# Performance work log

Hardware: AMD Instinct MI355X
Metric: run time of the kernel (lower is better)

## Reference

```python
import jax, jax.numpy as jnp
import numpy as np

BLOCK_SIZE = 256
N_EMBD = 256
HEAD_SIZE = 64


def setup_inputs() -> dict:
    key = jax.random.key(0)
    k1, k2, k3, k4, k5 = jax.random.split(key, 5)
    B, T = 256, 256
    x = jax.random.normal(k1, (B, T, N_EMBD), dtype=jnp.float32)
    # nn.Linear(n_embd, head_size, bias=False) weights, stored as [in, out] for x @ W
    s = 1.0 / np.sqrt(N_EMBD)
    Wk = jax.random.uniform(k2, (N_EMBD, HEAD_SIZE), minval=-s, maxval=s, dtype=jnp.float32)
    Wq = jax.random.uniform(k3, (N_EMBD, HEAD_SIZE), minval=-s, maxval=s, dtype=jnp.float32)
    Wv = jax.random.uniform(k4, (N_EMBD, HEAD_SIZE), minval=-s, maxval=s, dtype=jnp.float32)
    rel_pos_embedding = 0.02 * jax.random.normal(k5, (2 * BLOCK_SIZE - 1, HEAD_SIZE), dtype=jnp.float32)
    return {"x": x, "Wk": Wk, "Wq": Wq, "Wv": Wv, "rel_pos_embedding": rel_pos_embedding}


def reference(x, Wk, Wq, Wv, rel_pos_embedding):
    B, T, C = x.shape
    H = Wk.shape[-1]
    k = x @ Wk  # [B,T,H]
    q = x @ Wq  # [B,T,H]
    v = x @ Wv  # [B,T,H]
    # content scores (scaled); note: position scores are NOT scaled, matching original
    content = jnp.einsum('bth,bsh->bts', q, k) * (H ** -0.5)  # [B,T,T]
    # relative position indices: j - i + (block_size - 1)
    idx = jnp.arange(T)[None, :] - jnp.arange(T)[:, None] + (BLOCK_SIZE - 1)  # [T,T]
    rel_emb = rel_pos_embedding[idx]  # [T,T,H]
    position = jnp.einsum('bth,tsh->bts', q, rel_emb)  # [B,T,T]
    wei = content + position
    causal = jnp.tril(jnp.ones((T, T), dtype=bool))
    wei = jnp.where(causal[None, :, :], wei, -jnp.inf)
    wei = jax.nn.softmax(wei, axis=-1)
    # dropout omitted (eval mode / deterministic reference)
    out = jnp.einsum('bts,bsh->bth', wei, v)  # [B,T,H]
    return out
```

## Files before the change

### kernel.cpp

```cpp
#include <hip/hip_runtime.h>

#define BB 256
#define TT 256
#define CC 256
#define HH 64

typedef _Float16 half8 __attribute__((ext_vector_type(8)));
typedef _Float16 half4 __attribute__((ext_vector_type(4)));
typedef __fp16 fp16x2 __attribute__((ext_vector_type(2)));
typedef float floatx4 __attribute__((ext_vector_type(4)));

__global__ __launch_bounds__(256) void prep(
    const float* __restrict__ rpe,
    const float* __restrict__ Wk, const float* __restrict__ Wq, const float* __restrict__ Wv,
    _Float16* __restrict__ rpeh, _Float16* __restrict__ WT)
{
    const int bid = blockIdx.x, tid = threadIdx.x;
    if (bid < 64) {
        const int i = bid * 256 + tid;
        rpeh[i] = (_Float16)rpe[i];
    } else {
        const int wsel = (bid - 64) >> 6;
        const int n    = (bid - 64) & 63;
        const float* W = wsel == 0 ? Wk : (wsel == 1 ? Wq : Wv);
        WT[(size_t)(wsel * 64 + n) * 256 + tid] = (_Float16)W[tid * HH + n];
    }
}

__device__ __forceinline__ int slot_width(int w) {
    const int j = w >> 1;
    return (j < 2) ? 72 : (32 * j + 40);
}
__device__ __forceinline__ int slot_off(int w) {
    const int j = w >> 1;
    const int V = (j < 2) ? 72 : (32 * j + 40);
    const int S = (j == 0) ? 0 : (j == 1) ? 72 : (16 * j * j + 24 * j + 32);
    return 32 * S + (w & 1) * 16 * V;
}

__global__ __launch_bounds__(1024, 4) void fused(
    const float* __restrict__ x, const _Float16* __restrict__ WT,
    const _Float16* __restrict__ rpeh, float* __restrict__ out)
{
    __shared__ _Float16 lds[75264];
    _Float16* Klds = lds;
    _Float16* VT   = lds + 18432;
    _Float16* pool = lds + 35328;

    const int tid  = threadIdx.x;
    const int b    = blockIdx.x;
    const int w    = tid >> 6;
    const int lane = tid & 63;
    const int quad = lane >> 4;
    const int l    = lane & 15;

    union H8 { half8 v; fp16x2 p[4]; };
    const float4* xg = reinterpret_cast<const float4*>(x);
    const int row0g = b * 256 + w * 16;

    floatx4 acc[12];
#pragma unroll
    for (int nt = 0; nt < 12; ++nt) acc[nt] = (floatx4){0.f, 0.f, 0.f, 0.f};

#pragma unroll
    for (int c = 0; c < 2; ++c) {
#pragma unroll
        for (int i = 0; i < 3; ++i) {
            const int gi  = tid + i * 1024;
            const int row = gi >> 4;
            const int g   = gi & 15;
            *(half8*)&pool[row * 136 + g * 8] =
                *(const half8*)(WT + (size_t)row * 256 + c * 128 + g * 8);
        }
        __syncthreads();

        float4 xa[4][2];
#pragma unroll
        for (int kk = 0; kk < 4; ++kk) {
            const size_t base = (size_t)(row0g + l) * 64 + c * 32 + kk * 8 + quad * 2;
            xa[kk][0] = xg[base];
            xa[kk][1] = xg[base + 1];
        }
#pragma unroll
        for (int kk = 0; kk < 4; ++kk) {
            H8 u;
            u.p[0] = __builtin_amdgcn_cvt_pkrtz(xa[kk][0].x, xa[kk][0].y);
            u.p[1] = __builtin_amdgcn_cvt_pkrtz(xa[kk][0].z, xa[kk][0].w);
            u.p[2] = __builtin_amdgcn_cvt_pkrtz(xa[kk][1].x, xa[kk][1].y);
            u.p[3] = __builtin_amdgcn_cvt_pkrtz(xa[kk][1].z, xa[kk][1].w);
#pragma unroll
            for (int nt = 0; nt < 12; ++nt) {
                const half8 bf = *(const half8*)&pool[(nt * 16 + l) * 136 + kk * 32 + quad * 8];
                acc[nt] = __builtin_amdgcn_mfma_f32_16x16x32_f16(u.v, bf, acc[nt], 0, 0, 0);
            }
        }
        __syncthreads();
    }

    {
        const int trw = w * 16;
#pragma unroll
        for (int nt = 0; nt < 4; ++nt) {
#pragma unroll
            for (int r = 0; r < 4; ++r)
                Klds[(trw + quad * 4 + r) * 72 + nt * 16 + l] = (_Float16)(acc[nt][r] * 0.125f);
            half4 vv;
            vv[0] = (_Float16)acc[nt + 8][0];
            vv[1] = (_Float16)acc[nt + 8][1];
            vv[2] = (_Float16)acc[nt + 8][2];
            vv[3] = (_Float16)acc[nt + 8][3];
            *(half4*)&VT[(nt * 16 + l) * 264 + trw + quad * 4] = vv;
        }
    }
    __syncthreads();

    _Float16* wh = pool + slot_off(w);
    const int Vw = slot_width(w);
    const int tile  = w;
    const int tw    = tile * 16;
    const int stmax = tile;
    const int cmax  = tile >> 1;
    const int dtmin = 15 - tile;

    half8 qf0, qf1;
    {
#pragma unroll
        for (int nt = 0; nt < 4; ++nt)
#pragma unroll
            for (int r = 0; r < 4; ++r)
                wh[(quad * 4 + r) * Vw + nt * 16 + l] = (_Float16)acc[nt + 4][r];
        qf0 = *(const half8*)&wh[l * Vw + quad * 8];
        qf1 = *(const half8*)&wh[l * Vw + 32 + quad * 8];
    }

#pragma unroll
    for (int dt = 0; dt < 16; ++dt) {
        if (dt >= dtmin) {
            const _Float16* rp = rpeh + (size_t)(dt * 16 + l) * HH + quad * 8;
            const half8 bf0 = *(const half8*)rp;
            const half8 bf1 = *(const half8*)(rp + 32);
            floatx4 z = {0.f, 0.f, 0.f, 0.f};
            z = __builtin_amdgcn_mfma_f32_16x16x32_f16(qf0, bf0, z, 0, 0, 0);
            const floatx4 pacc = __builtin_amdgcn_mfma_f32_16x16x32_f16(qf1, bf1, z, 0, 0, 0);
            if (dt == dtmin) {
#pragma unroll
                for (int r = 0; r < 4; ++r) {
                    const int row = quad * 4 + r;
                    const int s   = l + row - 15;
                    if (s >= 0) wh[row * Vw + s] = (_Float16)pacc[r];
                }
            } else {
#pragma unroll
                for (int r = 0; r < 4; ++r) {
                    const int row = quad * 4 + r;
                    const int s   = dt * 16 + l + tw + row - 255;
                    wh[row * Vw + s] = (_Float16)pacc[r];
                }
            }
        }
    }

    floatx4 sacc[16];
#pragma unroll
    for (int st = 0; st < 16; ++st) {
        if (st <= stmax) {
            const _Float16* kp = &Klds[(st * 16 + l) * 72 + quad * 8];
            const half8 kf0 = *(const half8*)kp;
            const half8 kf1 = *(const half8*)(kp + 32);
            floatx4 z = {0.f, 0.f, 0.f, 0.f};
            z = __builtin_amdgcn_mfma_f32_16x16x32_f16(qf0, kf0, z, 0, 0, 0);
            sacc[st] = __builtin_amdgcn_mfma_f32_16x16x32_f16(qf1, kf1, z, 0, 0, 0);
        }
    }

    float sums[4] = {0.f, 0.f, 0.f, 0.f};
#pragma unroll
    for (int st = 0; st < 16; ++st) {
        if (st < stmax) {
            const int s = l + 16 * st;
#pragma unroll
            for (int r = 0; r < 4; ++r) {
                const int row = quad * 4 + r;
                const float e = __expf(sacc[st][r] + (float)wh[row * Vw + s]);
                sums[r] += e;
                wh[row * Vw + s] = (_Float16)e;
            }
        }
    }
    {
        const int s = l + 16 * stmax;
#pragma unroll
        for (int r = 0; r < 4; ++r) {
            const int row = quad * 4 + r;
            float e = 0.f;
            if (l <= row) e = __expf(sacc[stmax][r] + (float)wh[row * Vw + s]);
            sums[r] += e;
            wh[row * Vw + s] = (_Float16)e;
        }
    }
    if ((tile & 1) == 0) {
        const int s = l + 16 * (stmax + 1);
#pragma unroll
        for (int r = 0; r < 4; ++r) wh[(quad * 4 + r) * Vw + s] = (_Float16)0.f;
    }

    float inv_r[4];
#pragma unroll
    for (int r = 0; r < 4; ++r) {
        float sum = sums[r];
        sum += __shfl_xor(sum, 1);
        sum += __shfl_xor(sum, 2);
        sum += __shfl_xor(sum, 4);
        sum += __shfl_xor(sum, 8);
        inv_r[r] = 1.0f / sum;
    }

    floatx4 oacc[4] = {{0.f,0.f,0.f,0.f},{0.f,0.f,0.f,0.f},
                       {0.f,0.f,0.f,0.f},{0.f,0.f,0.f,0.f}};
#pragma unroll
    for (int c = 0; c < 8; ++c) {
        if (c <= cmax) {
            const half8 af = *(const half8*)&wh[l * Vw + c * 32 + quad * 8];
#pragma unroll
            for (int ht = 0; ht < 4; ++ht) {
                const half8 vf = *(const half8*)&VT[(ht * 16 + l) * 264 + c * 32 + quad * 8];
                oacc[ht] = __builtin_amdgcn_mfma_f32_16x16x32_f16(af, vf, oacc[ht], 0, 0, 0);
            }
        }
    }

#pragma unroll
    for (int ht = 0; ht < 4; ++ht) {
#pragma unroll
        for (int r = 0; r < 4; ++r) {
            const int t = tw + quad * 4 + r;
            out[(size_t)(b * TT + t) * HH + ht * 16 + l] = oacc[ht][r] * inv_r[r];
        }
    }
}

extern "C" void kernel_launch(void* const* d_in, const int* in_sizes, int n_in,
                              void* d_out, int out_size, void* d_ws, size_t ws_size,
                              hipStream_t stream) {
    const float* x   = (const float*)d_in[0];
    const float* Wk  = (const float*)d_in[1];
    const float* Wq  = (const float*)d_in[2];
    const float* Wv  = (const float*)d_in[3];
    const float* rpe = (const float*)d_in[4];
    float* out = (float*)d_out;

    _Float16* rpeh = (_Float16*)d_ws;
    _Float16* WT   = rpeh + 256 * HH;

    prep<<<dim3(256), dim3(256), 0, stream>>>(rpe, Wk, Wq, Wv, rpeh, WT);
    fused<<<dim3(BB), dim3(1024), 0, stream>>>(x, WT, rpeh, out);
}
```

Baseline: 131.9 us.

## Balance causal attention work across waves by splitting long query tiles

Reassigns the triangular causal workload so each wave processes its own tile up to nine key tiles and, for waves 0-7, also the tail key tiles of the mirrored long tile 15-w. Partial row sums are exchanged through a small shared array, and the PV stage is redistributed so each wave handles two head-column tiles for a short/long tile pair. This targets load imbalance where wave 15 did roughly sixteen times the work of wave 0, at the cost of extra barriers and shared-memory traffic.

```diff
diff --git a/kernel.cpp b/kernel.cpp
--- a/kernel.cpp
+++ b/kernel.cpp
@@ -27,15 +27,15 @@
     }
 }
 
-__device__ __forceinline__ int slot_width(int w) {
-    const int j = w >> 1;
+__device__ __forceinline__ int slot_width(int t) {
+    const int j = t >> 1;
     return (j < 2) ? 72 : (32 * j + 40);
 }
-__device__ __forceinline__ int slot_off(int w) {
-    const int j = w >> 1;
+__device__ __forceinline__ int slot_off(int t) {
+    const int j = t >> 1;
     const int V = (j < 2) ? 72 : (32 * j + 40);
     const int S = (j == 0) ? 0 : (j == 1) ? 72 : (16 * j * j + 24 * j + 32);
-    return 32 * S + (w & 1) * 16 * V;
+    return 32 * S + (t & 1) * 16 * V;
 }
 
 __global__ __launch_bounds__(1024, 4) void fused(
@@ -43,6 +43,7 @@
     const _Float16* __restrict__ rpeh, float* __restrict__ out)
 {
     __shared__ _Float16 lds[75264];
+    __shared__ float rowsumP[2][256];
     _Float16* Klds = lds;
     _Float16* VT   = lds + 18432;
     _Float16* pool = lds + 35328;
@@ -112,37 +113,42 @@
             *(half4*)&VT[(nt * 16 + l) * 264 + trw + quad * 4] = vv;
         }
     }
+    if (tid < 512) ((float*)rowsumP)[tid] = 0.f;
     __syncthreads();
 
     _Float16* wh = pool + slot_off(w);
     const int Vw = slot_width(w);
-    const int tile  = w;
-    const int tw    = tile * 16;
-    const int stmax = tile;
-    const int cmax  = tile >> 1;
-    const int dtmin = 15 - tile;
-
-    half8 qf0, qf1;
-    {
-#pragma unroll
-        for (int nt = 0; nt < 4; ++nt)
-#pragma unroll
-            for (int r = 0; r < 4; ++r)
-                wh[(quad * 4 + r) * Vw + nt * 16 + l] = (_Float16)acc[nt + 4][r];
-        qf0 = *(const half8*)&wh[l * Vw + quad * 8];
-        qf1 = *(const half8*)&wh[l * Vw + 32 + quad * 8];
-    }
-
-#pragma unroll
-    for (int dt = 0; dt < 16; ++dt) {
-        if (dt >= dtmin) {
+#pragma unroll
+    for (int nt = 0; nt < 4; ++nt)
+#pragma unroll
+        for (int r = 0; r < 4; ++r)
+            wh[(quad * 4 + r) * Vw + nt * 16 + l] = (_Float16)acc[nt + 4][r];
+    __syncthreads();
+
+    const half8 qf0 = *(const half8*)&wh[l * Vw + quad * 8];
+    const half8 qf1 = *(const half8*)&wh[l * Vw + 32 + quad * 8];
+    const int tp = 15 - w;
+    _Float16* whp = pool + slot_off(tp);
+    const int Vp = slot_width(tp);
+    half8 qg0 = qf0, qg1 = qf1;
+    if (w < 8) {
+        qg0 = *(const half8*)&whp[l * Vp + quad * 8];
+        qg1 = *(const half8*)&whp[l * Vp + 32 + quad * 8];
+    }
+    __syncthreads();
+
+    const int jmaxo = (w < 8) ? w : 8;
+#pragma unroll
+    for (int j = 0; j < 9; ++j) {
+        if (j <= jmaxo) {
+            const int dt = j + 15 - w;
             const _Float16* rp = rpeh + (size_t)(dt * 16 + l) * HH + quad * 8;
             const half8 bf0 = *(const half8*)rp;
             const half8 bf1 = *(const half8*)(rp + 32);
             floatx4 z = {0.f, 0.f, 0.f, 0.f};
             z = __builtin_amdgcn_mfma_f32_16x16x32_f16(qf0, bf0, z, 0, 0, 0);
             const floatx4 pacc = __builtin_amdgcn_mfma_f32_16x16x32_f16(qf1, bf1, z, 0, 0, 0);
-            if (dt == dtmin) {
+            if (j == 0) {
 #pragma unroll
                 for (int r = 0; r < 4; ++r) {
                     const int row = quad * 4 + r;
@@ -153,88 +159,161 @@
 #pragma unroll
                 for (int r = 0; r < 4; ++r) {
                     const int row = quad * 4 + r;
-                    const int s   = dt * 16 + l + tw + row - 255;
-                    wh[row * Vw + s] = (_Float16)pacc[r];
-                }
-            }
-        }
-    }
-
-    floatx4 sacc[16];
-#pragma unroll
-    for (int st = 0; st < 16; ++st) {
-        if (st <= stmax) {
-            const _Float16* kp = &Klds[(st * 16 + l) * 72 + quad * 8];
-            const half8 kf0 = *(const half8*)kp;
-            const half8 kf1 = *(const half8*)(kp + 32);
-            floatx4 z = {0.f, 0.f, 0.f, 0.f};
-            z = __builtin_amdgcn_mfma_f32_16x16x32_f16(qf0, kf0, z, 0, 0, 0);
-            sacc[st] = __builtin_amdgcn_mfma_f32_16x16x32_f16(qf1, kf1, z, 0, 0, 0);
-        }
-    }
-
-    float sums[4] = {0.f, 0.f, 0.f, 0.f};
-#pragma unroll
-    for (int st = 0; st < 16; ++st) {
-        if (st < stmax) {
-            const int s = l + 16 * st;
+                    wh[row * Vw + 16 * j + l + row - 15] = (_Float16)pacc[r];
+                }
+            }
+        }
+    }
+    if (w < 8) {
+#pragma unroll
+        for (int j = 9; j < 16; ++j) {
+            if (j <= 15 - w) {
+                const int dt = j + w;
+                const _Float16* rp = rpeh + (size_t)(dt * 16 + l) * HH + quad * 8;
+                const half8 bf0 = *(const half8*)rp;
+                const half8 bf1 = *(const half8*)(rp + 32);
+                floatx4 z = {0.f, 0.f, 0.f, 0.f};
+                z = __builtin_amdgcn_mfma_f32_16x16x32_f16(qg0, bf0, z, 0, 0, 0);
+                const floatx4 pacc = __builtin_amdgcn_mfma_f32_16x16x32_f16(qg1, bf1, z, 0, 0, 0);
+#pragma unroll
+                for (int r = 0; r < 4; ++r) {
+                    const int row = quad * 4 + r;
+                    whp[row * Vp + 16 * j + l + row - 15] = (_Float16)pacc[r];
+                }
+            }
+        }
+    }
+    __syncthreads();
+
+    {
+        float sumsA[4] = {0.f, 0.f, 0.f, 0.f};
+#pragma unroll
+        for (int st = 0; st < 9; ++st) {
+            if (st <= jmaxo) {
+                const _Float16* kp = &Klds[(st * 16 + l) * 72 + quad * 8];
+                const half8 kf0 = *(const half8*)kp;
+                const half8 kf1 = *(const half8*)(kp + 32);
+                floatx4 z = {0.f, 0.f, 0.f, 0.f};
+                z = __builtin_amdgcn_mfma_f32_16x16x32_f16(qf0, kf0, z, 0, 0, 0);
+                const floatx4 sacc = __builtin_amdgcn_mfma_f32_16x16x32_f16(qf1, kf1, z, 0, 0, 0);
+                const int s = l + 16 * st;
+                if (st == w) {
+#pragma unroll
+                    for (int r = 0; r < 4; ++r) {
+                        const int row = quad * 4 + r;
+                        float e = 0.f;
+                        if (l <= row) e = __expf(sacc[r] + (float)wh[row * Vw + s]);
+                        sumsA[r] += e;
+                        wh[row * Vw + s] = (_Float16)e;
+                    }
+                    if ((w & 1) == 0) {
+                        const int s2 = l + 16 * (st + 1);
+#pragma unroll
+                        for (int r = 0; r < 4; ++r) wh[(quad * 4 + r) * Vw + s2] = (_Float16)0.f;
+                    }
+                } else {
+#pragma unroll
+                    for (int r = 0; r < 4; ++r) {
+                        const int row = quad * 4 + r;
+                        const float e = __expf(sacc[r] + (float)wh[row * Vw + s]);
+                        sumsA[r] += e;
+                        wh[row * Vw + s] = (_Float16)e;
+                    }
+                }
+            }
+        }
+#pragma unroll
+        for (int r = 0; r < 4; ++r) {
+            float sv = sumsA[r];
+            sv += __shfl_xor(sv, 1);
+            sv += __shfl_xor(sv, 2);
+            sv += __shfl_xor(sv, 4);
+            sv += __shfl_xor(sv, 8);
+            if (l == 0) rowsumP[0][16 * w + quad * 4 + r] = sv;
+        }
+    }
+    if (w < 8) {
+        float sumsB[4] = {0.f, 0.f, 0.f, 0.f};
+#pragma unroll
+        for (int st = 9; st < 16; ++st) {
+            if (st <= 15 - w) {
+                const _Float16* kp = &Klds[(st * 16 + l) * 72 + quad * 8];
+                const half8 kf0 = *(const half8*)kp;
+                const half8 kf1 = *(const half8*)(kp + 32);
+                floatx4 z = {0.f, 0.f, 0.f, 0.f};
+                z = __builtin_amdgcn_mfma_f32_16x16x32_f16(qg0, kf0, z, 0, 0, 0);
+                const floatx4 sacc = __builtin_amdgcn_mfma_f32_16x16x32_f16(qg1, kf1, z, 0, 0, 0);
+                const int s = l + 16 * st;
+                if (st == tp) {
+#pragma unroll
+                    for (int r = 0; r < 4; ++r) {
+                        const int row = quad * 4 + r;
+                        float e = 0.f;
+                        if (l <= row) e = __expf(sacc[r] + (float)whp[row * Vp + s]);
+                        sumsB[r] += e;
+                        whp[row * Vp + s] = (_Float16)e;
+                    }
+                    if ((tp & 1) == 0) {
+                        const int s2 = l + 16 * (st + 1);
+#pragma unroll
+                        for (int r = 0; r < 4; ++r) whp[(quad * 4 + r) * Vp + s2] = (_Float16)0.f;
+                    }
+                } else {
+#pragma unroll
+                    for (int r = 0; r < 4; ++r) {
+                        const int row = quad * 4 + r;
+                        const float e = __expf(sacc[r] + (float)whp[row * Vp + s]);
+                        sumsB[r] += e;
+                        whp[row * Vp + s] = (_Float16)e;
+                    }
+                }
+            }
+        }
+#pragma unroll
+        for (int r = 0; r < 4; ++r) {
+            float sv = sumsB[r];
+            sv += __shfl_xor(sv, 1);
+            sv += __shfl_xor(sv, 2);
+            sv += __shfl_xor(sv, 4);
+            sv += __shfl_xor(sv, 8);
+            if (l == 0) rowsumP[1][16 * tp + quad * 4 + r] = sv;
+        }
+    }
+    __syncthreads();
+
+    {
+        const int t1 = w >> 1;
+        const int hb = (w & 1) << 1;
+#pragma unroll
+        for (int sel = 0; sel < 2; ++sel) {
+            const int tt = sel ? (15 - t1) : t1;
+            const _Float16* ws = pool + slot_off(tt);
+            const int Vt    = slot_width(tt);
+            const int cmaxt = tt >> 1;
+            float inv[4];
 #pragma unroll
             for (int r = 0; r < 4; ++r) {
-                const int row = quad * 4 + r;
-                const float e = __expf(sacc[st][r] + (float)wh[row * Vw + s]);
-                sums[r] += e;
-                wh[row * Vw + s] = (_Float16)e;
-            }
-        }
-    }
-    {
-        const int s = l + 16 * stmax;
-#pragma unroll
-        for (int r = 0; r < 4; ++r) {
-            const int row = quad * 4 + r;
-            float e = 0.f;
-            if (l <= row) e = __expf(sacc[stmax][r] + (float)wh[row * Vw + s]);
-            sums[r] += e;
-            wh[row * Vw + s] = (_Float16)e;
-        }
-    }
-    if ((tile & 1) == 0) {
-        const int s = l + 16 * (stmax + 1);
-#pragma unroll
-        for (int r = 0; r < 4; ++r) wh[(quad * 4 + r) * Vw + s] = (_Float16)0.f;
-    }
-
-    float inv_r[4];
-#pragma unroll
-    for (int r = 0; r < 4; ++r) {
-        float sum = sums[r];
-        sum += __shfl_xor(sum, 1);
-        sum += __shfl_xor(sum, 2);
-        sum += __shfl_xor(sum, 4);
-        sum += __shfl_xor(sum, 8);
-        inv_r[r] = 1.0f / sum;
-    }
-
-    floatx4 oacc[4] = {{0.f,0.f,0.f,0.f},{0.f,0.f,0.f,0.f},
-                       {0.f,0.f,0.f,0.f},{0.f,0.f,0.f,0.f}};
-#pragma unroll
-    for (int c = 0; c < 8; ++c) {
-        if (c <= cmax) {
-            const half8 af = *(const half8*)&wh[l * Vw + c * 32 + quad * 8];
-#pragma unroll
-            for (int ht = 0; ht < 4; ++ht) {
-                const half8 vf = *(const half8*)&VT[(ht * 16 + l) * 264 + c * 32 + quad * 8];
-                oacc[ht] = __builtin_amdgcn_mfma_f32_16x16x32_f16(af, vf, oacc[ht], 0, 0, 0);
-            }
-        }
-    }
-
-#pragma unroll
-    for (int ht = 0; ht < 4; ++ht) {
-#pragma unroll
-        for (int r = 0; r < 4; ++r) {
-            const int t = tw + quad * 4 + r;
-            out[(size_t)(b * TT + t) * HH + ht * 16 + l] = oacc[ht][r] * inv_r[r];
+                const int row = 16 * tt + quad * 4 + r;
+                inv[r] = 1.0f / (rowsumP[0][row] + rowsumP[1][row]);
+            }
+            floatx4 o0 = {0.f, 0.f, 0.f, 0.f};
+            floatx4 o1 = {0.f, 0.f, 0.f, 0.f};
+#pragma unroll
+            for (int c = 0; c < 8; ++c) {
+                if (c <= cmaxt) {
+                    const half8 af  = *(const half8*)&ws[l * Vt + c * 32 + quad * 8];
+                    const half8 vf0 = *(const half8*)&VT[((hb + 0) * 16 + l) * 264 + c * 32 + quad * 8];
+                    const half8 vf1 = *(const half8*)&VT[((hb + 1) * 16 + l) * 264 + c * 32 + quad * 8];
+                    o0 = __builtin_amdgcn_mfma_f32_16x16x32_f16(af, vf0, o0, 0, 0, 0);
+                    o1 = __builtin_amdgcn_mfma_f32_16x16x32_f16(af, vf1, o1, 0, 0, 0);
+                }
+            }
+#pragma unroll
+            for (int r = 0; r < 4; ++r) {
+                const int t = 16 * tt + quad * 4 + r;
+                out[(size_t)(b * TT + t) * HH + (hb + 0) * 16 + l] = o0[r] * inv[r];
+                out[(size_t)(b * TT + t) * HH + (hb + 1) * 16 + l] = o1[r] * inv[r];
+            }
         }
     }
 }
```

Result: faster. 123.5 us (-6.3%).

## Split each batch into two 512-thread query-half blocks with streamed K/V chunks

Applied to the files above, without the earlier changes.

Each batch's 256 query rows are now split across two blocks of 8 waves (512 blocks total). The first half-block recomputes K/V only for rows 0-127, and the second recomputes all 256 rows. K/V chunks of 64 rows are written into double-buffered, XOR-swizzled LDS tiles, while position and content scores are computed per chunk into a small per-wave slot. The aim is to cut LDS footprint, raise occupancy, and spread the causal workload across more CUs. The cost is redundant K/V projection for the first 128 rows and one extra barrier per chunk.

```diff
diff --git a/kernel.cpp b/kernel.cpp
--- a/kernel.cpp
+++ b/kernel.cpp
@@ -2,11 +2,10 @@
 
 #define BB 256
 #define TT 256
-#define CC 256
 #define HH 64
 
 typedef _Float16 half8 __attribute__((ext_vector_type(8)));
-typedef _Float16 half4 __attribute__((ext_vector_type(4)));
+typedef _Float16 half4v __attribute__((ext_vector_type(4)));
 typedef __fp16 fp16x2 __attribute__((ext_vector_type(2)));
 typedef float floatx4 __attribute__((ext_vector_type(4)));
 
@@ -27,216 +26,259 @@
     }
 }
 
-__device__ __forceinline__ int slot_width(int w) {
-    const int j = w >> 1;
-    return (j < 2) ? 72 : (32 * j + 40);
-}
-__device__ __forceinline__ int slot_off(int w) {
-    const int j = w >> 1;
-    const int V = (j < 2) ? 72 : (32 * j + 40);
-    const int S = (j == 0) ? 0 : (j == 1) ? 72 : (16 * j * j + 24 * j + 32);
-    return 32 * S + (w & 1) * 16 * V;
-}
-
-__global__ __launch_bounds__(1024, 4) void fused(
+__device__ __forceinline__ half8 cvt8(const float4& a, const float4& b) {
+    union H8 { half8 v; fp16x2 p[4]; } u;
+    u.p[0] = __builtin_amdgcn_cvt_pkrtz(a.x, a.y);
+    u.p[1] = __builtin_amdgcn_cvt_pkrtz(a.z, a.w);
+    u.p[2] = __builtin_amdgcn_cvt_pkrtz(b.x, b.y);
+    u.p[3] = __builtin_amdgcn_cvt_pkrtz(b.z, b.w);
+    return u.v;
+}
+
+template<int H>
+__device__ __forceinline__ void run_half(
     const float* __restrict__ x, const _Float16* __restrict__ WT,
-    const _Float16* __restrict__ rpeh, float* __restrict__ out)
+    const _Float16* __restrict__ rpeh, float* __restrict__ out,
+    _Float16* lds, const int b, const int tid)
 {
-    __shared__ _Float16 lds[75264];
-    _Float16* Klds = lds;
-    _Float16* VT   = lds + 18432;
-    _Float16* pool = lds + 35328;
-
-    const int tid  = threadIdx.x;
-    const int b    = blockIdx.x;
+    constexpr int RPW = 16 << H;
+    constexpr int NRT = 1 << H;
+    constexpr int NCH = 2 + 2 * H;
+    constexpr int WPC = 4 >> H;
+
+    _Float16* Kbuf = lds;
+    _Float16* Vbuf = lds + 8192;
+    _Float16* pool = lds + 16384;
+
     const int w    = tid >> 6;
     const int lane = tid & 63;
     const int quad = lane >> 4;
     const int l    = lane & 15;
-
-    union H8 { half8 v; fp16x2 p[4]; };
+    const int t    = 8 * H + w;
+
     const float4* xg = reinterpret_cast<const float4*>(x);
-    const int row0g = b * 256 + w * 16;
-
-    floatx4 acc[12];
-#pragma unroll
-    for (int nt = 0; nt < 12; ++nt) acc[nt] = (floatx4){0.f, 0.f, 0.f, 0.f};
-
-#pragma unroll
-    for (int c = 0; c < 2; ++c) {
-#pragma unroll
-        for (int i = 0; i < 3; ++i) {
-            const int gi  = tid + i * 1024;
-            const int row = gi >> 4;
-            const int g   = gi & 15;
-            *(half8*)&pool[row * 136 + g * 8] =
-                *(const half8*)(WT + (size_t)row * 256 + c * 128 + g * 8);
+    const int kvrow = b * 256 + RPW * w;
+    const int qrow  = b * 256 + 16 * t;
+
+    floatx4 akv[NRT][8];
+    floatx4 aq[4];
+#pragma unroll
+    for (int rt = 0; rt < NRT; ++rt)
+#pragma unroll
+        for (int nt = 0; nt < 8; ++nt) akv[rt][nt] = (floatx4){0.f,0.f,0.f,0.f};
+#pragma unroll
+    for (int nt = 0; nt < 4; ++nt) aq[nt] = (floatx4){0.f,0.f,0.f,0.f};
+
+#pragma unroll
+    for (int kc = 0; kc < 2; ++kc) {
+#pragma unroll
+        for (int i = 0; i < 6; ++i) {
+            const int gi = tid + i * 512, row = gi >> 4, g = gi & 15;
+            *(half8*)&lds[row * 136 + g * 8] =
+                *(const half8*)(WT + (size_t)row * 256 + kc * 128 + g * 8);
         }
         __syncthreads();
 
-        float4 xa[4][2];
-#pragma unroll
-        for (int kk = 0; kk < 4; ++kk) {
-            const size_t base = (size_t)(row0g + l) * 64 + c * 32 + kk * 8 + quad * 2;
-            xa[kk][0] = xg[base];
-            xa[kk][1] = xg[base + 1];
-        }
-#pragma unroll
-        for (int kk = 0; kk < 4; ++kk) {
-            H8 u;
-            u.p[0] = __builtin_amdgcn_cvt_pkrtz(xa[kk][0].x, xa[kk][0].y);
-            u.p[1] = __builtin_amdgcn_cvt_pkrtz(xa[kk][0].z, xa[kk][0].w);
-            u.p[2] = __builtin_amdgcn_cvt_pkrtz(xa[kk][1].x, xa[kk][1].y);
-            u.p[3] = __builtin_amdgcn_cvt_pkrtz(xa[kk][1].z, xa[kk][1].w);
-#pragma unroll
-            for (int nt = 0; nt < 12; ++nt) {
-                const half8 bf = *(const half8*)&pool[(nt * 16 + l) * 136 + kk * 32 + quad * 8];
-                acc[nt] = __builtin_amdgcn_mfma_f32_16x16x32_f16(u.v, bf, acc[nt], 0, 0, 0);
+#pragma unroll
+        for (int rt = 0; rt < NRT; ++rt) {
+            const size_t xb = (size_t)(kvrow + rt * 16 + l) * 64 + kc * 32 + quad * 2;
+            float4 a0 = xg[xb], a1 = xg[xb + 1];
+#pragma unroll
+            for (int kk = 0; kk < 4; ++kk) {
+                float4 n0, n1;
+                if (kk < 3) { n0 = xg[xb + (kk + 1) * 8]; n1 = xg[xb + (kk + 1) * 8 + 1]; }
+                const half8 u = cvt8(a0, a1);
+#pragma unroll
+                for (int nt = 0; nt < 4; ++nt) {
+                    const half8 bk = *(const half8*)&lds[(nt * 16 + l) * 136 + kk * 32 + quad * 8];
+                    akv[rt][nt] = __builtin_amdgcn_mfma_f32_16x16x32_f16(u, bk, akv[rt][nt], 0, 0, 0);
+                }
+#pragma unroll
+                for (int nt = 0; nt < 4; ++nt) {
+                    const half8 bv = *(const half8*)&lds[(128 + nt * 16 + l) * 136 + kk * 32 + quad * 8];
+                    akv[rt][4 + nt] = __builtin_amdgcn_mfma_f32_16x16x32_f16(u, bv, akv[rt][4 + nt], 0, 0, 0);
+                }
+                a0 = n0; a1 = n1;
+            }
+        }
+        {
+            const size_t xb = (size_t)(qrow + l) * 64 + kc * 32 + quad * 2;
+#pragma unroll
+            for (int kk = 0; kk < 4; ++kk) {
+                const float4 a0 = xg[xb + kk * 8], a1 = xg[xb + kk * 8 + 1];
+                const half8 u = cvt8(a0, a1);
+#pragma unroll
+                for (int nt = 0; nt < 4; ++nt) {
+                    const half8 bq = *(const half8*)&lds[(64 + nt * 16 + l) * 136 + kk * 32 + quad * 8];
+                    aq[nt] = __builtin_amdgcn_mfma_f32_16x16x32_f16(u, bq, aq[nt], 0, 0, 0);
+                }
             }
         }
         __syncthreads();
     }
 
-    {
-        const int trw = w * 16;
-#pragma unroll
-        for (int nt = 0; nt < 4; ++nt) {
-#pragma unroll
-            for (int r = 0; r < 4; ++r)
-                Klds[(trw + quad * 4 + r) * 72 + nt * 16 + l] = (_Float16)(acc[nt][r] * 0.125f);
-            half4 vv;
-            vv[0] = (_Float16)acc[nt + 8][0];
-            vv[1] = (_Float16)acc[nt + 8][1];
-            vv[2] = (_Float16)acc[nt + 8][2];
-            vv[3] = (_Float16)acc[nt + 8][3];
-            *(half4*)&VT[(nt * 16 + l) * 264 + trw + quad * 4] = vv;
-        }
-    }
+    half4v kp[NRT][4], vp[NRT][4];
+#pragma unroll
+    for (int rt = 0; rt < NRT; ++rt)
+#pragma unroll
+        for (int nt = 0; nt < 4; ++nt)
+#pragma unroll
+            for (int r = 0; r < 4; ++r) {
+                kp[rt][nt][r] = (_Float16)(akv[rt][nt][r] * 0.125f);
+                vp[rt][nt][r] = (_Float16)akv[rt][4 + nt][r];
+            }
+
+    _Float16* wh = pool + w * 1088;
+#pragma unroll
+    for (int nt = 0; nt < 4; ++nt)
+#pragma unroll
+        for (int r = 0; r < 4; ++r)
+            wh[(quad * 4 + r) * 68 + nt * 16 + l] = (_Float16)aq[nt][r];
+    const half8 qf0 = *(const half8*)&wh[l * 68 + quad * 8];
+    const half8 qf1 = *(const half8*)&wh[l * 68 + 32 + quad * 8];
+
+    auto write_chunk = [&](int cn) {
+        char* Kb = (char*)(Kbuf + (cn & 1) * 4096);
+        char* Vb = (char*)(Vbuf + (cn & 1) * 4096);
+        const int lr0 = (w - WPC * cn) * RPW;
+#pragma unroll
+        for (int rt = 0; rt < NRT; ++rt) {
+            const int rb = lr0 + rt * 16;
+#pragma unroll
+            for (int nt = 0; nt < 4; ++nt) {
+#pragma unroll
+                for (int r = 0; r < 4; ++r) {
+                    const int rr  = rb + quad * 4 + r;
+                    const int off = (rr * 128 + (nt * 16 + l) * 2) ^ (((quad * 4 + r) & 7) << 4);
+                    *(_Float16*)(Kb + off) = kp[rt][nt][r];
+                }
+                const int voff = ((nt * 16 + l) * 128 + (rb + quad * 4) * 2) ^ ((l & 7) << 4);
+                *(half4v*)(Vb + voff) = vp[rt][nt];
+            }
+        }
+    };
+
+    if (w < WPC) write_chunk(0);
     __syncthreads();
 
-    _Float16* wh = pool + slot_off(w);
-    const int Vw = slot_width(w);
-    const int tile  = w;
-    const int tw    = tile * 16;
-    const int stmax = tile;
-    const int cmax  = tile >> 1;
-    const int dtmin = 15 - tile;
-
-    half8 qf0, qf1;
-    {
-#pragma unroll
-        for (int nt = 0; nt < 4; ++nt)
-#pragma unroll
-            for (int r = 0; r < 4; ++r)
-                wh[(quad * 4 + r) * Vw + nt * 16 + l] = (_Float16)acc[nt + 4][r];
-        qf0 = *(const half8*)&wh[l * Vw + quad * 8];
-        qf1 = *(const half8*)&wh[l * Vw + 32 + quad * 8];
-    }
-
-#pragma unroll
-    for (int dt = 0; dt < 16; ++dt) {
-        if (dt >= dtmin) {
-            const _Float16* rp = rpeh + (size_t)(dt * 16 + l) * HH + quad * 8;
-            const half8 bf0 = *(const half8*)rp;
-            const half8 bf1 = *(const half8*)(rp + 32);
-            floatx4 z = {0.f, 0.f, 0.f, 0.f};
-            z = __builtin_amdgcn_mfma_f32_16x16x32_f16(qf0, bf0, z, 0, 0, 0);
-            const floatx4 pacc = __builtin_amdgcn_mfma_f32_16x16x32_f16(qf1, bf1, z, 0, 0, 0);
-            if (dt == dtmin) {
-#pragma unroll
-                for (int r = 0; r < 4; ++r) {
-                    const int row = quad * 4 + r;
-                    const int s   = l + row - 15;
-                    if (s >= 0) wh[row * Vw + s] = (_Float16)pacc[r];
-                }
-            } else {
-#pragma unroll
-                for (int r = 0; r < 4; ++r) {
-                    const int row = quad * 4 + r;
-                    const int s   = dt * 16 + l + tw + row - 255;
-                    wh[row * Vw + s] = (_Float16)pacc[r];
-                }
-            }
-        }
-    }
-
-    floatx4 sacc[16];
-#pragma unroll
-    for (int st = 0; st < 16; ++st) {
-        if (st <= stmax) {
-            const _Float16* kp = &Klds[(st * 16 + l) * 72 + quad * 8];
-            const half8 kf0 = *(const half8*)kp;
-            const half8 kf1 = *(const half8*)(kp + 32);
-            floatx4 z = {0.f, 0.f, 0.f, 0.f};
-            z = __builtin_amdgcn_mfma_f32_16x16x32_f16(qf0, kf0, z, 0, 0, 0);
-            sacc[st] = __builtin_amdgcn_mfma_f32_16x16x32_f16(qf1, kf1, z, 0, 0, 0);
-        }
-    }
-
     float sums[4] = {0.f, 0.f, 0.f, 0.f};
-#pragma unroll
-    for (int st = 0; st < 16; ++st) {
-        if (st < stmax) {
-            const int s = l + 16 * st;
-#pragma unroll
-            for (int r = 0; r < 4; ++r) {
-                const int row = quad * 4 + r;
-                const float e = __expf(sacc[st][r] + (float)wh[row * Vw + s]);
-                sums[r] += e;
-                wh[row * Vw + s] = (_Float16)e;
-            }
-        }
-    }
-    {
-        const int s = l + 16 * stmax;
-#pragma unroll
-        for (int r = 0; r < 4; ++r) {
-            const int row = quad * 4 + r;
-            float e = 0.f;
-            if (l <= row) e = __expf(sacc[stmax][r] + (float)wh[row * Vw + s]);
-            sums[r] += e;
-            wh[row * Vw + s] = (_Float16)e;
-        }
-    }
-    if ((tile & 1) == 0) {
-        const int s = l + 16 * (stmax + 1);
-#pragma unroll
-        for (int r = 0; r < 4; ++r) wh[(quad * 4 + r) * Vw + s] = (_Float16)0.f;
-    }
-
-    float inv_r[4];
-#pragma unroll
-    for (int r = 0; r < 4; ++r) {
-        float sum = sums[r];
-        sum += __shfl_xor(sum, 1);
-        sum += __shfl_xor(sum, 2);
-        sum += __shfl_xor(sum, 4);
-        sum += __shfl_xor(sum, 8);
-        inv_r[r] = 1.0f / sum;
-    }
-
     floatx4 oacc[4] = {{0.f,0.f,0.f,0.f},{0.f,0.f,0.f,0.f},
                        {0.f,0.f,0.f,0.f},{0.f,0.f,0.f,0.f}};
-#pragma unroll
-    for (int c = 0; c < 8; ++c) {
+    const int cmax = t >> 2;
+    const int xorv = (l & 7) << 4;
+
+    for (int c = 0; c < NCH; ++c) {
+        if (c + 1 < NCH && (unsigned)(w - WPC * (c + 1)) < (unsigned)WPC)
+            write_chunk(c + 1);
+
         if (c <= cmax) {
-            const half8 af = *(const half8*)&wh[l * Vw + c * 32 + quad * 8];
-#pragma unroll
-            for (int ht = 0; ht < 4; ++ht) {
-                const half8 vf = *(const half8*)&VT[(ht * 16 + l) * 264 + c * 32 + quad * 8];
-                oacc[ht] = __builtin_amdgcn_mfma_f32_16x16x32_f16(af, vf, oacc[ht], 0, 0, 0);
-            }
-        }
-    }
-
-#pragma unroll
-    for (int ht = 0; ht < 4; ++ht) {
-#pragma unroll
-        for (int r = 0; r < 4; ++r) {
-            const int t = tw + quad * 4 + r;
-            out[(size_t)(b * TT + t) * HH + ht * 16 + l] = oacc[ht][r] * inv_r[r];
-        }
-    }
+            char* Kb = (char*)(Kbuf + (c & 1) * 4096);
+            char* Vb = (char*)(Vbuf + (c & 1) * 4096);
+            const int tl = t - 4 * c;
+            const int stmaxl = tl < 3 ? tl : 3;
+
+#pragma unroll
+            for (int sl = 0; sl <= 4; ++sl) {
+                const int st = 4 * c + sl;
+                if (st <= t) {
+                    const int dt = st - t + 15;
+                    const _Float16* rp = rpeh + (size_t)(dt * 16 + l) * 64 + quad * 8;
+                    const half8 b0 = *(const half8*)rp;
+                    const half8 b1 = *(const half8*)(rp + 32);
+                    floatx4 z = {0.f,0.f,0.f,0.f};
+                    z = __builtin_amdgcn_mfma_f32_16x16x32_f16(qf0, b0, z, 0, 0, 0);
+                    const floatx4 pa = __builtin_amdgcn_mfma_f32_16x16x32_f16(qf1, b1, z, 0, 0, 0);
+#pragma unroll
+                    for (int r = 0; r < 4; ++r) {
+                        const int row = quad * 4 + r;
+                        const int col = 16 * sl + l + row - 15;
+                        if (sl == 0)      { if (col >= 0) wh[row * 68 + col] = (_Float16)pa[r]; }
+                        else if (sl == 4) { if (col < 64) wh[row * 68 + col] = (_Float16)pa[r]; }
+                        else                wh[row * 68 + col] = (_Float16)pa[r];
+                    }
+                }
+            }
+
+#pragma unroll
+            for (int sl = 0; sl < 4; ++sl) {
+                if (sl <= stmaxl) {
+                    const int st = 4 * c + sl;
+                    const int rbyte = (sl * 16 + l) * 128;
+                    const half8 k0 = *(const half8*)(Kb + ((rbyte + quad * 16) ^ xorv));
+                    const half8 k1 = *(const half8*)(Kb + ((rbyte + 64 + quad * 16) ^ xorv));
+                    floatx4 z = {0.f,0.f,0.f,0.f};
+                    z = __builtin_amdgcn_mfma_f32_16x16x32_f16(qf0, k0, z, 0, 0, 0);
+                    const floatx4 sa = __builtin_amdgcn_mfma_f32_16x16x32_f16(qf1, k1, z, 0, 0, 0);
+                    const int scol = 16 * sl + l;
+                    if (st == t) {
+#pragma unroll
+                        for (int r = 0; r < 4; ++r) {
+                            const int row = quad * 4 + r;
+                            float e = 0.f;
+                            if (l <= row) e = __expf(sa[r] + (float)wh[row * 68 + scol]);
+                            sums[r] += e;
+                            wh[row * 68 + scol] = (_Float16)e;
+                        }
+                    } else {
+#pragma unroll
+                        for (int r = 0; r < 4; ++r) {
+                            const int row = quad * 4 + r;
+                            const float e = __expf(sa[r] + (float)wh[row * 68 + scol]);
+                            sums[r] += e;
+                            wh[row * 68 + scol] = (_Float16)e;
+                        }
+                    }
+                }
+            }
+            if (c == cmax && (stmaxl & 1) == 0) {
+                const int zc = 16 * (stmaxl + 1) + l;
+#pragma unroll
+                for (int r = 0; r < 4; ++r) wh[(quad * 4 + r) * 68 + zc] = (_Float16)0.f;
+            }
+
+            const int c2max = stmaxl >> 1;
+#pragma unroll
+            for (int c2 = 0; c2 < 2; ++c2) {
+                if (c2 <= c2max) {
+                    const half8 af = *(const half8*)&wh[l * 68 + c2 * 32 + quad * 8];
+#pragma unroll
+                    for (int ht = 0; ht < 4; ++ht) {
+                        const int vo = ((ht * 16 + l) * 128 + c2 * 64 + quad * 16) ^ xorv;
+                        const half8 vf = *(const half8*)(Vb + vo);
+                        oacc[ht] = __builtin_amdgcn_mfma_f32_16x16x32_f16(af, vf, oacc[ht], 0, 0, 0);
+                    }
+                }
+            }
+        }
+        __syncthreads();
+    }
+
+    float inv[4];
+#pragma unroll
+    for (int r = 0; r < 4; ++r) {
+        float sv = sums[r];
+        sv += __shfl_xor(sv, 1);
+        sv += __shfl_xor(sv, 2);
+        sv += __shfl_xor(sv, 4);
+        sv += __shfl_xor(sv, 8);
+        inv[r] = 1.0f / sv;
+    }
+#pragma unroll
+    for (int ht = 0; ht < 4; ++ht)
+#pragma unroll
+        for (int r = 0; r < 4; ++r)
+            out[(size_t)(qrow + quad * 4 + r) * 64 + ht * 16 + l] = oacc[ht][r] * inv[r];
+}
+
+__global__ __launch_bounds__(512, 4) void fused(
+    const float* __restrict__ x, const _Float16* __restrict__ WT,
+    const _Float16* __restrict__ rpeh, float* __restrict__ out)
+{
+    __shared__ _Float16 lds[26112];
+    const int h = blockIdx.x >> 8;
+    const int b = blockIdx.x & 255;
+    if (h == 0) run_half<0>(x, WT, rpeh, out, lds, b, threadIdx.x);
+    else        run_half<1>(x, WT, rpeh, out, lds, b, threadIdx.x);
 }
 
 extern "C" void kernel_launch(void* const* d_in, const int* in_sizes, int n_in,
@@ -253,5 +295,5 @@
     _Float16* WT   = rpeh + 256 * HH;
 
     prep<<<dim3(256), dim3(256), 0, stream>>>(rpe, Wk, Wq, Wv, rpeh, WT);
-    fused<<<dim3(BB), dim3(1024), 0, stream>>>(x, WT, rpeh, out);
-}
+    fused<<<dim3(512), dim3(512), 0, stream>>>(x, WT, rpeh, out);
+}
```

After: 180.9 us. +37.1%, slower.

## Balance causal attention work across waves and keep scores in registers

Applied to the files above, without the earlier changes.

Causal work is rebalanced so each low wave also handles the upper half of the key range for its mirror tile (15-w), and partial outputs and row sums are merged through LDS. Scores are computed transposed (K as A operand) and exponentiated straight into packed fp16 registers, then shuffled into the PV MFMA operand, so the probabilities no longer round-trip through LDS. The projection now stages both halves of the weights at once with one barrier instead of two per chunk, and the K row stride is padded from 72 to 76. The aim is to remove load imbalance between waves and the LDS traffic for P, at the cost of more shuffles, extra barriers and added register pressure.

```diff
diff --git a/kernel.cpp b/kernel.cpp
--- a/kernel.cpp
+++ b/kernel.cpp
@@ -2,7 +2,6 @@
 
 #define BB 256
 #define TT 256
-#define CC 256
 #define HH 64
 
 typedef _Float16 half8 __attribute__((ext_vector_type(8)));
@@ -27,25 +26,72 @@
     }
 }
 
-__device__ __forceinline__ int slot_width(int w) {
-    const int j = w >> 1;
+__device__ __forceinline__ int slot_width(int t) {
+    const int j = t >> 1;
     return (j < 2) ? 72 : (32 * j + 40);
 }
-__device__ __forceinline__ int slot_off(int w) {
-    const int j = w >> 1;
+__device__ __forceinline__ int slot_off(int t) {
+    const int j = t >> 1;
     const int V = (j < 2) ? 72 : (32 * j + 40);
     const int S = (j == 0) ? 0 : (j == 1) ? 72 : (16 * j * j + 24 * j + 32);
-    return 32 * S + (w & 1) * 16 * V;
+    return 32 * S + (t & 1) * 16 * V;
+}
+
+__device__ __forceinline__ void score_exp(
+    const _Float16* __restrict__ Klds, const _Float16* __restrict__ slot,
+    int Vs, int st, int diagSt, int l, int quad,
+    half8 qa, half8 qb, float& sum, unsigned& pk0, unsigned& pk1)
+{
+    const _Float16* kp = &Klds[(st * 16 + l) * 76 + quad * 8];
+    const half8 kf0 = *(const half8*)kp;
+    const half8 kf1 = *(const half8*)(kp + 32);
+    floatx4 z = {0.f, 0.f, 0.f, 0.f};
+    z = __builtin_amdgcn_mfma_f32_16x16x32_f16(kf0, qa, z, 0, 0, 0);
+    const floatx4 sa = __builtin_amdgcn_mfma_f32_16x16x32_f16(kf1, qb, z, 0, 0, 0);
+    const half4 ph = *(const half4*)&slot[l * Vs + st * 16 + quad * 4];
+    const bool dg = (st == diagSt);
+    const float e0 = (!dg || 4 * quad + 0 <= l) ? __expf(sa[0] + (float)ph[0]) : 0.f;
+    const float e1 = (!dg || 4 * quad + 1 <= l) ? __expf(sa[1] + (float)ph[1]) : 0.f;
+    const float e2 = (!dg || 4 * quad + 2 <= l) ? __expf(sa[2] + (float)ph[2]) : 0.f;
+    const float e3 = (!dg || 4 * quad + 3 <= l) ? __expf(sa[3] + (float)ph[3]) : 0.f;
+    sum += e0 + e1 + e2 + e3;
+    union { fp16x2 h; unsigned u; } ua, ub;
+    ua.h = __builtin_amdgcn_cvt_pkrtz(e0, e1);
+    ub.h = __builtin_amdgcn_cvt_pkrtz(e2, e3);
+    pk0 = ua.u; pk1 = ub.u;
+}
+
+__device__ __forceinline__ void pv_chunk(
+    const _Float16* __restrict__ VT, int c, int l, int quad, int srcA, bool hi2,
+    unsigned p10, unsigned p11, unsigned p20, unsigned p21, floatx4* oa)
+{
+    const unsigned a0 = (unsigned)__shfl((int)p10, srcA);
+    const unsigned a1 = (unsigned)__shfl((int)p11, srcA);
+    const unsigned a2 = (unsigned)__shfl((int)p10, srcA + 16);
+    const unsigned a3 = (unsigned)__shfl((int)p11, srcA + 16);
+    const unsigned b0 = (unsigned)__shfl((int)p20, srcA);
+    const unsigned b1 = (unsigned)__shfl((int)p21, srcA);
+    const unsigned b2 = (unsigned)__shfl((int)p20, srcA + 16);
+    const unsigned b3 = (unsigned)__shfl((int)p21, srcA + 16);
+    union { unsigned u[4]; half8 v; } pb;
+    pb.u[0] = hi2 ? b0 : a0; pb.u[1] = hi2 ? b1 : a1;
+    pb.u[2] = hi2 ? b2 : a2; pb.u[3] = hi2 ? b3 : a3;
+#pragma unroll
+    for (int ht = 0; ht < 4; ++ht) {
+        const half8 vf = *(const half8*)&VT[(ht * 16 + l) * 264 + c * 32 + quad * 8];
+        oa[ht] = __builtin_amdgcn_mfma_f32_16x16x32_f16(vf, pb.v, oa[ht], 0, 0, 0);
+    }
 }
 
 __global__ __launch_bounds__(1024, 4) void fused(
     const float* __restrict__ x, const _Float16* __restrict__ WT,
     const _Float16* __restrict__ rpeh, float* __restrict__ out)
 {
-    __shared__ _Float16 lds[75264];
+    __shared__ _Float16 lds[76288];
+    __shared__ float rowsumP[256];
     _Float16* Klds = lds;
-    _Float16* VT   = lds + 18432;
-    _Float16* pool = lds + 35328;
+    _Float16* VT   = lds + 19456;
+    _Float16* pool = lds + 36352;
 
     const int tid  = threadIdx.x;
     const int b    = blockIdx.x;
@@ -62,24 +108,31 @@
 #pragma unroll
     for (int nt = 0; nt < 12; ++nt) acc[nt] = (floatx4){0.f, 0.f, 0.f, 0.f};
 
-#pragma unroll
-    for (int c = 0; c < 2; ++c) {
+    {
 #pragma unroll
         for (int i = 0; i < 3; ++i) {
             const int gi  = tid + i * 1024;
             const int row = gi >> 4;
             const int g   = gi & 15;
-            *(half8*)&pool[row * 136 + g * 8] =
-                *(const half8*)(WT + (size_t)row * 256 + c * 128 + g * 8);
-        }
-        __syncthreads();
-
+            const _Float16* src = WT + (size_t)row * 256 + g * 8;
+            *(half8*)&pool[row * 136 + g * 8] = *(const half8*)src;
+            *(half8*)&lds[row * 136 + g * 8]  = *(const half8*)(src + 128);
+        }
         float4 xa[4][2];
 #pragma unroll
         for (int kk = 0; kk < 4; ++kk) {
-            const size_t base = (size_t)(row0g + l) * 64 + c * 32 + kk * 8 + quad * 2;
+            const size_t base = (size_t)(row0g + l) * 64 + kk * 8 + quad * 2;
             xa[kk][0] = xg[base];
             xa[kk][1] = xg[base + 1];
+        }
+        __syncthreads();
+
+        float4 xb[4][2];
+#pragma unroll
+        for (int kk = 0; kk < 4; ++kk) {
+            const size_t base = (size_t)(row0g + l) * 64 + 32 + kk * 8 + quad * 2;
+            xb[kk][0] = xg[base];
+            xb[kk][1] = xg[base + 1];
         }
 #pragma unroll
         for (int kk = 0; kk < 4; ++kk) {
@@ -94,16 +147,33 @@
                 acc[nt] = __builtin_amdgcn_mfma_f32_16x16x32_f16(u.v, bf, acc[nt], 0, 0, 0);
             }
         }
+#pragma unroll
+        for (int kk = 0; kk < 4; ++kk) {
+            H8 u;
+            u.p[0] = __builtin_amdgcn_cvt_pkrtz(xb[kk][0].x, xb[kk][0].y);
+            u.p[1] = __builtin_amdgcn_cvt_pkrtz(xb[kk][0].z, xb[kk][0].w);
+            u.p[2] = __builtin_amdgcn_cvt_pkrtz(xb[kk][1].x, xb[kk][1].y);
+            u.p[3] = __builtin_amdgcn_cvt_pkrtz(xb[kk][1].z, xb[kk][1].w);
+#pragma unroll
+            for (int nt = 0; nt < 12; ++nt) {
+                const half8 bf = *(const half8*)&lds[(nt * 16 + l) * 136 + kk * 32 + quad * 8];
+                acc[nt] = __builtin_amdgcn_mfma_f32_16x16x32_f16(u.v, bf, acc[nt], 0, 0, 0);
+            }
+        }
         __syncthreads();
     }
 
+    _Float16* wh = pool + slot_off(w);
+    const int Vw = slot_width(w);
     {
         const int trw = w * 16;
 #pragma unroll
         for (int nt = 0; nt < 4; ++nt) {
 #pragma unroll
-            for (int r = 0; r < 4; ++r)
-                Klds[(trw + quad * 4 + r) * 72 + nt * 16 + l] = (_Float16)(acc[nt][r] * 0.125f);
+            for (int r = 0; r < 4; ++r) {
+                Klds[(trw + quad * 4 + r) * 76 + nt * 16 + l] = (_Float16)(acc[nt][r] * 0.125f);
+                wh[(quad * 4 + r) * Vw + nt * 16 + l] = (_Float16)acc[nt + 4][r];
+            }
             half4 vv;
             vv[0] = (_Float16)acc[nt + 8][0];
             vv[1] = (_Float16)acc[nt + 8][1];
@@ -114,128 +184,125 @@
     }
     __syncthreads();
 
-    _Float16* wh = pool + slot_off(w);
-    const int Vw = slot_width(w);
-    const int tile  = w;
-    const int tw    = tile * 16;
-    const int stmax = tile;
-    const int cmax  = tile >> 1;
-    const int dtmin = 15 - tile;
-
-    half8 qf0, qf1;
-    {
-#pragma unroll
-        for (int nt = 0; nt < 4; ++nt)
-#pragma unroll
-            for (int r = 0; r < 4; ++r)
-                wh[(quad * 4 + r) * Vw + nt * 16 + l] = (_Float16)acc[nt + 4][r];
-        qf0 = *(const half8*)&wh[l * Vw + quad * 8];
-        qf1 = *(const half8*)&wh[l * Vw + 32 + quad * 8];
-    }
-
-#pragma unroll
-    for (int dt = 0; dt < 16; ++dt) {
-        if (dt >= dtmin) {
+    const half8 qf0 = *(const half8*)&wh[l * Vw + quad * 8];
+    const half8 qf1 = *(const half8*)&wh[l * Vw + 32 + quad * 8];
+    const int tp = 15 - w;
+    _Float16* whp = pool + slot_off(tp);
+    const int Vp = slot_width(tp);
+    half8 qg0 = qf0, qg1 = qf1;
+    if (w < 8) {
+        qg0 = *(const half8*)&whp[l * Vp + quad * 8];
+        qg1 = *(const half8*)&whp[l * Vp + 32 + quad * 8];
+    }
+    __syncthreads();
+
+    const int jmaxo = (w < 8) ? w : 8;
+#pragma unroll
+    for (int j = 0; j < 9; ++j) {
+        if (j <= jmaxo) {
+            const int dt = j + 15 - w;
             const _Float16* rp = rpeh + (size_t)(dt * 16 + l) * HH + quad * 8;
             const half8 bf0 = *(const half8*)rp;
             const half8 bf1 = *(const half8*)(rp + 32);
             floatx4 z = {0.f, 0.f, 0.f, 0.f};
             z = __builtin_amdgcn_mfma_f32_16x16x32_f16(qf0, bf0, z, 0, 0, 0);
             const floatx4 pacc = __builtin_amdgcn_mfma_f32_16x16x32_f16(qf1, bf1, z, 0, 0, 0);
-            if (dt == dtmin) {
+#pragma unroll
+            for (int r = 0; r < 4; ++r) {
+                const int row = quad * 4 + r;
+                const int s   = 16 * j + l + row - 15;
+                if (j == 0)      { if (s >= 0) wh[row * Vw + s] = (_Float16)pacc[r]; }
+                else if (j == 8) { if (l + row <= 14) wh[row * Vw + s] = (_Float16)pacc[r]; }
+                else               wh[row * Vw + s] = (_Float16)pacc[r];
+            }
+        }
+    }
+    if (w < 8) {
+#pragma unroll
+        for (int j = 8; j < 16; ++j) {
+            if (j <= tp) {
+                const int dt = j + w;
+                const _Float16* rp = rpeh + (size_t)(dt * 16 + l) * HH + quad * 8;
+                const half8 bf0 = *(const half8*)rp;
+                const half8 bf1 = *(const half8*)(rp + 32);
+                floatx4 z = {0.f, 0.f, 0.f, 0.f};
+                z = __builtin_amdgcn_mfma_f32_16x16x32_f16(qg0, bf0, z, 0, 0, 0);
+                const floatx4 pacc = __builtin_amdgcn_mfma_f32_16x16x32_f16(qg1, bf1, z, 0, 0, 0);
 #pragma unroll
                 for (int r = 0; r < 4; ++r) {
                     const int row = quad * 4 + r;
-                    const int s   = l + row - 15;
-                    if (s >= 0) wh[row * Vw + s] = (_Float16)pacc[r];
+                    const int s   = 16 * j + l + row - 15;
+                    if (j == 8) { if (l + row >= 15) whp[row * Vp + s] = (_Float16)pacc[r]; }
+                    else          whp[row * Vp + s] = (_Float16)pacc[r];
                 }
-            } else {
-#pragma unroll
-                for (int r = 0; r < 4; ++r) {
-                    const int row = quad * 4 + r;
-                    const int s   = dt * 16 + l + tw + row - 255;
-                    wh[row * Vw + s] = (_Float16)pacc[r];
-                }
-            }
-        }
-    }
-
-    floatx4 sacc[16];
-#pragma unroll
-    for (int st = 0; st < 16; ++st) {
-        if (st <= stmax) {
-            const _Float16* kp = &Klds[(st * 16 + l) * 72 + quad * 8];
-            const half8 kf0 = *(const half8*)kp;
-            const half8 kf1 = *(const half8*)(kp + 32);
-            floatx4 z = {0.f, 0.f, 0.f, 0.f};
-            z = __builtin_amdgcn_mfma_f32_16x16x32_f16(qf0, kf0, z, 0, 0, 0);
-            sacc[st] = __builtin_amdgcn_mfma_f32_16x16x32_f16(qf1, kf1, z, 0, 0, 0);
-        }
-    }
-
-    float sums[4] = {0.f, 0.f, 0.f, 0.f};
-#pragma unroll
-    for (int st = 0; st < 16; ++st) {
-        if (st < stmax) {
-            const int s = l + 16 * st;
-#pragma unroll
-            for (int r = 0; r < 4; ++r) {
-                const int row = quad * 4 + r;
-                const float e = __expf(sacc[st][r] + (float)wh[row * Vw + s]);
-                sums[r] += e;
-                wh[row * Vw + s] = (_Float16)e;
-            }
-        }
-    }
-    {
-        const int s = l + 16 * stmax;
-#pragma unroll
-        for (int r = 0; r < 4; ++r) {
-            const int row = quad * 4 + r;
-            float e = 0.f;
-            if (l <= row) e = __expf(sacc[stmax][r] + (float)wh[row * Vw + s]);
-            sums[r] += e;
-            wh[row * Vw + s] = (_Float16)e;
-        }
-    }
-    if ((tile & 1) == 0) {
-        const int s = l + 16 * (stmax + 1);
-#pragma unroll
-        for (int r = 0; r < 4; ++r) wh[(quad * 4 + r) * Vw + s] = (_Float16)0.f;
-    }
-
-    float inv_r[4];
-#pragma unroll
-    for (int r = 0; r < 4; ++r) {
-        float sum = sums[r];
-        sum += __shfl_xor(sum, 1);
-        sum += __shfl_xor(sum, 2);
-        sum += __shfl_xor(sum, 4);
-        sum += __shfl_xor(sum, 8);
-        inv_r[r] = 1.0f / sum;
-    }
-
+            }
+        }
+    }
+
+    const int srcA = l + ((quad & 1) << 5);
+    const bool hi2 = (quad >= 2);
+    float sumO = 0.f;
     floatx4 oacc[4] = {{0.f,0.f,0.f,0.f},{0.f,0.f,0.f,0.f},
                        {0.f,0.f,0.f,0.f},{0.f,0.f,0.f,0.f}};
-#pragma unroll
-    for (int c = 0; c < 8; ++c) {
-        if (c <= cmax) {
-            const half8 af = *(const half8*)&wh[l * Vw + c * 32 + quad * 8];
-#pragma unroll
-            for (int ht = 0; ht < 4; ++ht) {
-                const half8 vf = *(const half8*)&VT[(ht * 16 + l) * 264 + c * 32 + quad * 8];
-                oacc[ht] = __builtin_amdgcn_mfma_f32_16x16x32_f16(af, vf, oacc[ht], 0, 0, 0);
-            }
-        }
-    }
-
+    const int stmaxO = (w < 8) ? w : 7;
+#pragma unroll
+    for (int c = 0; c < 4; ++c) {
+        if (c <= (stmaxO >> 1)) {
+            unsigned p10, p11, p20 = 0u, p21 = 0u;
+            score_exp(Klds, wh, Vw, 2 * c, w, l, quad, qf0, qf1, sumO, p10, p11);
+            if (2 * c + 1 <= stmaxO)
+                score_exp(Klds, wh, Vw, 2 * c + 1, w, l, quad, qf0, qf1, sumO, p20, p21);
+            pv_chunk(VT, c, l, quad, srcA, hi2, p10, p11, p20, p21, oacc);
+        }
+    }
+    float sumP = 0.f;
+    floatx4 oaccP[4] = {{0.f,0.f,0.f,0.f},{0.f,0.f,0.f,0.f},
+                        {0.f,0.f,0.f,0.f},{0.f,0.f,0.f,0.f}};
+    if (w < 8) {
+#pragma unroll
+        for (int c = 4; c < 8; ++c) {
+            if (c <= (tp >> 1)) {
+                unsigned p10, p11, p20 = 0u, p21 = 0u;
+                score_exp(Klds, whp, Vp, 2 * c, tp, l, quad, qg0, qg1, sumP, p10, p11);
+                if (2 * c + 1 <= tp)
+                    score_exp(Klds, whp, Vp, 2 * c + 1, tp, l, quad, qg0, qg1, sumP, p20, p21);
+                pv_chunk(VT, c, l, quad, srcA, hi2, p10, p11, p20, p21, oaccP);
+            }
+        }
+        sumP += __shfl_xor(sumP, 16);
+        sumP += __shfl_xor(sumP, 32);
+    }
+    sumO += __shfl_xor(sumO, 16);
+    sumO += __shfl_xor(sumO, 32);
+
+    __syncthreads();
+    if (w < 8) {
+        float* ob = (float*)(pool + slot_off(tp));
+#pragma unroll
+        for (int ht = 0; ht < 4; ++ht)
+            *(floatx4*)&ob[l * 68 + ht * 16 + quad * 4] = oaccP[ht];
+        if (lane < 16) rowsumP[16 * tp + lane] = sumP;
+    }
+    __syncthreads();
+
+    float inv;
+    if (w >= 8) {
+        const float* ob = (const float*)(pool + slot_off(w));
+#pragma unroll
+        for (int ht = 0; ht < 4; ++ht)
+            oacc[ht] += *(const floatx4*)&ob[l * 68 + ht * 16 + quad * 4];
+        inv = 1.0f / (sumO + rowsumP[16 * w + l]);
+    } else {
+        inv = 1.0f / sumO;
+    }
 #pragma unroll
     for (int ht = 0; ht < 4; ++ht) {
-#pragma unroll
-        for (int r = 0; r < 4; ++r) {
-            const int t = tw + quad * 4 + r;
-            out[(size_t)(b * TT + t) * HH + ht * 16 + l] = oacc[ht][r] * inv_r[r];
-        }
+        float4 o;
+        o.x = oacc[ht][0] * inv;
+        o.y = oacc[ht][1] * inv;
+        o.z = oacc[ht][2] * inv;
+        o.w = oacc[ht][3] * inv;
+        *(float4*)&out[(size_t)(b * 256 + 16 * w + l) * 64 + ht * 16 + quad * 4] = o;
     }
 }
 
```

Result: faster. 128.4 us (-2.7%).
